# Kernel tuning notes

Measured on AMD Instinct MI355X. Metric: run time of the kernel, lower is better.

## Reference

```python
import jax, jax.numpy as jnp
import numpy as np

N_NODES = 100000
N_EDGES = 1600000
NFEAT = 128
NHID = 128
NCLASS = 40


def gcn_conv(x, W, b, src, dst, n_nodes):
    """PyG-style GCNConv: x' = D^{-1/2}(A+I)D^{-1/2} (x W) + b."""
    h = x @ W  # [N, out]
    loop = jnp.arange(n_nodes, dtype=src.dtype)
    s = jnp.concatenate([src, loop])  # add self-loops
    d = jnp.concatenate([dst, loop])
    deg = jax.ops.segment_sum(jnp.ones_like(s, dtype=h.dtype), d, num_segments=n_nodes)
    dinv = jnp.where(deg > 0, jax.lax.rsqrt(deg), 0.0)
    norm = dinv[s] * dinv[d]  # [E+N]
    msg = h[s] * norm[:, None]  # gather + scale
    out = jax.ops.segment_sum(msg, d, num_segments=n_nodes)  # scatter-add
    return out + b


def setup_inputs() -> dict:
    key = jax.random.key(0)
    ks = jax.random.split(key, 6)
    x = jax.random.normal(ks[0], (N_NODES, NFEAT), dtype=jnp.float32)
    edge_index = jax.random.randint(ks[1], (2, N_EDGES), 0, N_NODES, dtype=jnp.int64)
    sc1 = 1.0 / np.sqrt(NFEAT)
    sc2 = 1.0 / np.sqrt(NHID)
    W1 = jax.random.normal(ks[2], (NFEAT, NHID), dtype=jnp.float32) * sc1
    b1 = jnp.zeros((NHID,), dtype=jnp.float32)
    Wm = jax.random.normal(ks[3], (NHID, NHID), dtype=jnp.float32) * sc2
    bm = jnp.zeros((NHID,), dtype=jnp.float32)
    W2 = jax.random.normal(ks[4], (NHID, NCLASS), dtype=jnp.float32) * sc2
    b2 = jnp.zeros((NCLASS,), dtype=jnp.float32)
    return {"x": x, "edge_index": edge_index, "W1": W1, "b1": b1,
            "Wm": Wm, "bm": bm, "W2": W2, "b2": b2}


def reference(x, edge_index, W1, b1, Wm, bm, W2, b2):
    # StandGCNX forward, eval mode (dropout = identity)
    src, dst = edge_index[0], edge_index[1]
    n = x.shape[0]
    h = jax.nn.relu(gcn_conv(x, W1, b1, src, dst, n))
    h = jax.nn.relu(gcn_conv(h, Wm, bm, src, dst, n))
    out = gcn_conv(h, W2, b2, src, dst, n)
    return out
```

## Files before the change

### kernel.cpp

```cpp
#include <hip/hip_runtime.h>
#include <hip/hip_bf16.h>

typedef __attribute__((ext_vector_type(8))) short bf16x8;
typedef __attribute__((ext_vector_type(4))) float f32x4;

__device__ __forceinline__ ushort bf16rne(float f) {
    uint u = __float_as_uint(f);
    return (ushort)((u + 0x7fffu + ((u >> 16) & 1u)) >> 16);
}
__device__ __forceinline__ void unpack2(uint p, float& a, float& b) {
    a = __uint_as_float(p << 16);
    b = __uint_as_float(p & 0xffff0000u);
}


__global__ __launch_bounds__(256) void k_bhist(const int* __restrict__ dst,
                                               int* __restrict__ bcnt, int E) {
    __shared__ int hist[512];
    int t = threadIdx.x;
    hist[t] = 0; hist[t + 256] = 0;
    __syncthreads();
    int off = blockIdx.x * 4096;
    int cnt = min(4096, E - off);
    for (int i = t; i < cnt; i += 256) atomicAdd(&hist[dst[off + i] >> 8], 1);
    __syncthreads();
    if (hist[t]) atomicAdd(&bcnt[t], hist[t]);
    if (hist[t + 256]) atomicAdd(&bcnt[t + 256], hist[t + 256]);
}

__global__ void k_bscan(const int* __restrict__ bcnt, int* __restrict__ bbase,
                        int* __restrict__ bcur, int nbuck) {
    __shared__ int s[512];
    int t = threadIdx.x;
    s[t] = (t < nbuck) ? bcnt[t] : 0;
    __syncthreads();
    for (int d = 1; d < 512; d <<= 1) {
        int u = (t >= d) ? s[t - d] : 0;
        __syncthreads();
        if (t >= d) s[t] += u;
        __syncthreads();
    }
    int excl = (t == 0) ? 0 : s[t - 1];
    bbase[t] = excl;
    if (t < nbuck) bcur[t] = excl;
    if (t == 511) bbase[512] = s[511];
}

__global__ __launch_bounds__(256) void k_binpack(const int* __restrict__ src,
                                                 const int* __restrict__ dst,
                                                 int* __restrict__ bcur,
                                                 uint* __restrict__ pairbuf,
                                                 int E, int nbuck) {
    __shared__ int hist[512];
    __shared__ int scn[512];
    __shared__ int cur[512];
    __shared__ int gbase[512];
    __shared__ uint sorted[4096];
    int t = threadIdx.x;
    int off = blockIdx.x * 4096;
    int cnt = min(4096, E - off);

    hist[t] = 0; hist[t + 256] = 0;
    __syncthreads();
    for (int i = t; i < cnt; i += 256) {
        int b = dst[off + i] >> 8;
        atomicAdd(&hist[b], 1);
    }
    __syncthreads();
    scn[t] = hist[t]; scn[t + 256] = hist[t + 256];
    __syncthreads();
    for (int d = 1; d < 256; d <<= 1) {
        int u0 = (t >= d) ? scn[t - d] : 0;
        int u1 = (t >= d) ? scn[256 + t - d] : 0;
        __syncthreads();
        if (t >= d) { scn[t] += u0; scn[256 + t] += u1; }
        __syncthreads();
    }
    int tot0 = scn[255];
    scn[256 + t] += tot0;
    __syncthreads();
    cur[t] = (t == 0) ? 0 : scn[t - 1];
    cur[t + 256] = scn[t + 255];
    if (t < nbuck && hist[t] > 0) gbase[t] = atomicAdd(&bcur[t], hist[t]);
    int t2 = t + 256;
    if (t2 < nbuck && hist[t2] > 0) gbase[t2] = atomicAdd(&bcur[t2], hist[t2]);
    __syncthreads();
    for (int i = t; i < cnt; i += 256) {
        int d = dst[off + i];
        int s = src[off + i];
        int b = d >> 8;
        int pos = atomicAdd(&cur[b], 1);
        sorted[pos] = ((uint)(d & 255) << 24) | (uint)s;
    }
    __syncthreads();
    int wid = t >> 6, lane = t & 63;
    for (int b = wid; b < nbuck; b += 4) {
        int n = hist[b];
        if (n == 0) continue;
        int ls = (b == 0) ? 0 : scn[b - 1];
        int gb = gbase[b];
        for (int j = lane; j < n; j += 64)
            pairbuf[gb + j] = sorted[ls + j];
    }
}

#define CSR_CAP 5632
__global__ __launch_bounds__(256) void k_csrbuild(const uint* __restrict__ pairbuf,
                                                  const int* __restrict__ bbase,
                                                  int* __restrict__ rowptr,
                                                  float* __restrict__ dinv,
                                                  int* __restrict__ csr,
                                                  int N, int nbuck) {
    __shared__ int lhist[256];
    __shared__ int scn[256];
    __shared__ int lcur[256];
    __shared__ int lcsr[CSR_CAP];
    int b = blockIdx.x;
    int base = b << 8;
    int nn = min(256, N - base);
    int lo = bbase[b], hi = bbase[b + 1];
    int cnt = hi - lo;
    int t = threadIdx.x;
    lhist[t] = 0;
    __syncthreads();
    for (int i = t; i < cnt; i += 256) atomicAdd(&lhist[pairbuf[lo + i] >> 24], 1);
    __syncthreads();
    int mydeg = lhist[t];
    scn[t] = mydeg;
    __syncthreads();
    for (int d = 1; d < 256; d <<= 1) {
        int u = (t >= d) ? scn[t - d] : 0;
        __syncthreads();
        if (t >= d) scn[t] += u;
        __syncthreads();
    }
    int excl = (t == 0) ? 0 : scn[t - 1];
    lcur[t] = excl;
    if (t < nn) {
        rowptr[base + t] = lo + excl;
        dinv[base + t] = rsqrtf((float)(mydeg + 1));
    }
    if (b == nbuck - 1 && t == 0) rowptr[N] = hi;
    __syncthreads();
    if (cnt <= CSR_CAP) {
        for (int i = t; i < cnt; i += 256) {
            uint p = pairbuf[lo + i];
            int pos = atomicAdd(&lcur[p >> 24], 1);
            lcsr[pos] = (int)(p & 0xFFFFFFu);
        }
        __syncthreads();
        for (int i = t; i < cnt; i += 256) csr[lo + i] = lcsr[i];
    } else {
        for (int i = t; i < cnt; i += 256) {
            uint p = pairbuf[lo + i];
            int pos = lo + atomicAdd(&lcur[p >> 24], 1);
            csr[pos] = (int)(p & 0xFFFFFFu);
        }
    }
}


__global__ void k_castT_all(const float* __restrict__ W1, const float* __restrict__ Wm,
                            const float* __restrict__ W2, ushort* __restrict__ w1t,
                            ushort* __restrict__ wmt, ushort* __restrict__ w2t) {
    int b = blockIdx.x;
    int t = threadIdx.x;
    if (b < 64) {
        int i = b * 256 + t; int k = i >> 7, n = i & 127;
        w1t[n * 128 + k] = bf16rne(W1[k * 128 + n]);
    } else if (b < 128) {
        int i = (b - 64) * 256 + t; int k = i >> 7, n = i & 127;
        wmt[n * 128 + k] = bf16rne(Wm[k * 128 + n]);
    } else {
        int i = (b - 128) * 256 + t;
        if (i < 6144) {
            int n = i >> 7, k = i & 127;
            w2t[n * 128 + k] = (n < 40) ? bf16rne(W2[k * 40 + n]) : (ushort)0;
        }
    }
}


__global__ __launch_bounds__(256) void k_gemm1(const float* __restrict__ A,
                                               const ushort* __restrict__ Wt,
                                               const float* __restrict__ dinv,
                                               ushort* __restrict__ C, int M) {
    int t = threadIdx.x;
    int wave = t >> 6, lane = t & 63;
    int m16 = lane & 15, quad = lane >> 4;
    int rowA = blockIdx.x * 64 + wave * 16 + m16;
    int rA = min(rowA, M - 1);
    const float4* A4 = (const float4*)A;

    f32x4 acc[8];
#pragma unroll
    for (int i = 0; i < 8; i++) acc[i] = (f32x4){0.f, 0.f, 0.f, 0.f};

#pragma unroll
    for (int it = 0; it < 4; it++) {
        float4 f0 = A4[(size_t)rA * 32 + 8 * it + 2 * quad];
        float4 f1 = A4[(size_t)rA * 32 + 8 * it + 2 * quad + 1];
        bf16x8 af;
        af[0] = (short)bf16rne(f0.x); af[1] = (short)bf16rne(f0.y);
        af[2] = (short)bf16rne(f0.z); af[3] = (short)bf16rne(f0.w);
        af[4] = (short)bf16rne(f1.x); af[5] = (short)bf16rne(f1.y);
        af[6] = (short)bf16rne(f1.z); af[7] = (short)bf16rne(f1.w);
#pragma unroll
        for (int nt = 0; nt < 8; nt++) {
            bf16x8 bfr = *(const bf16x8*)(Wt + (size_t)(nt * 16 + m16) * 128 + it * 32 + quad * 8);
            acc[nt] = __builtin_amdgcn_mfma_f32_16x16x32_bf16(af, bfr, acc[nt], 0, 0, 0);
        }
    }
    int rowBase = blockIdx.x * 64 + wave * 16 + quad * 4;
    float dnv[4];
#pragma unroll
    for (int r = 0; r < 4; r++) dnv[r] = dinv[min(rowBase + r, M - 1)];
#pragma unroll
    for (int nt = 0; nt < 8; nt++) {
        int col = nt * 16 + m16;
#pragma unroll
        for (int r = 0; r < 4; r++) {
            int row = rowBase + r;
            if (row < M) C[(size_t)row * 128 + col] = bf16rne(acc[nt][r] * dnv[r]);
        }
    }
}


template <int NT>
__device__ __forceinline__ void fused_agg_gemm(const ushort* __restrict__ g,
                                               const float* __restrict__ dinv,
                                               const int* __restrict__ rowptr,
                                               const int* __restrict__ csr,
                                               const float* __restrict__ bias,
                                               const ushort* __restrict__ Wt,
                                               ushort* __restrict__ C,
                                               int M, int ccols) {
    int t = threadIdx.x;
    int wave = t >> 6, lane = t & 63;
    int m16 = lane & 15, quad = lane >> 4;
    int node = blockIdx.x * 64 + wave * 16 + m16;
    int nd = min(node, M - 1);
    const uint4* g16 = (const uint4*)g;
    float dn = dinv[nd];

    float a[4][8];
    {
#pragma unroll
        for (int it = 0; it < 4; it++) {
            uint4 p = g16[(size_t)nd * 16 + 4 * it + quad];
            unpack2(p.x, a[it][0], a[it][1]); unpack2(p.y, a[it][2], a[it][3]);
            unpack2(p.z, a[it][4], a[it][5]); unpack2(p.w, a[it][6], a[it][7]);
        }
    }
    int e0 = rowptr[nd], e1 = rowptr[nd + 1];
    int e = e0;
    for (; e + 2 <= e1; e += 2) {
        int s0 = csr[e], s1 = csr[e + 1];
        uint4 p0[4], p1[4];
#pragma unroll
        for (int it = 0; it < 4; it++) p0[it] = g16[(size_t)s0 * 16 + 4 * it + quad];
#pragma unroll
        for (int it = 0; it < 4; it++) p1[it] = g16[(size_t)s1 * 16 + 4 * it + quad];
        float u, v;
#pragma unroll
        for (int it = 0; it < 4; it++) {
            unpack2(p0[it].x, u, v); a[it][0] += u; a[it][1] += v;
            unpack2(p0[it].y, u, v); a[it][2] += u; a[it][3] += v;
            unpack2(p0[it].z, u, v); a[it][4] += u; a[it][5] += v;
            unpack2(p0[it].w, u, v); a[it][6] += u; a[it][7] += v;
            unpack2(p1[it].x, u, v); a[it][0] += u; a[it][1] += v;
            unpack2(p1[it].y, u, v); a[it][2] += u; a[it][3] += v;
            unpack2(p1[it].z, u, v); a[it][4] += u; a[it][5] += v;
            unpack2(p1[it].w, u, v); a[it][6] += u; a[it][7] += v;
        }
    }
    for (; e < e1; e++) {
        int s = csr[e];
        float u, v;
#pragma unroll
        for (int it = 0; it < 4; it++) {
            uint4 p = g16[(size_t)s * 16 + 4 * it + quad];
            unpack2(p.x, u, v); a[it][0] += u; a[it][1] += v;
            unpack2(p.y, u, v); a[it][2] += u; a[it][3] += v;
            unpack2(p.z, u, v); a[it][4] += u; a[it][5] += v;
            unpack2(p.w, u, v); a[it][6] += u; a[it][7] += v;
        }
    }
    const float4* b4 = (const float4*)bias;
    bf16x8 frag[4];
#pragma unroll
    for (int it = 0; it < 4; it++) {
        float4 bb0 = b4[8 * it + 2 * quad];
        float4 bb1 = b4[8 * it + 2 * quad + 1];
        float o0 = fmaxf(a[it][0] * dn + bb0.x, 0.f);
        float o1 = fmaxf(a[it][1] * dn + bb0.y, 0.f);
        float o2 = fmaxf(a[it][2] * dn + bb0.z, 0.f);
        float o3 = fmaxf(a[it][3] * dn + bb0.w, 0.f);
        float o4 = fmaxf(a[it][4] * dn + bb1.x, 0.f);
        float o5 = fmaxf(a[it][5] * dn + bb1.y, 0.f);
        float o6 = fmaxf(a[it][6] * dn + bb1.z, 0.f);
        float o7 = fmaxf(a[it][7] * dn + bb1.w, 0.f);
        frag[it][0] = (short)bf16rne(o0); frag[it][1] = (short)bf16rne(o1);
        frag[it][2] = (short)bf16rne(o2); frag[it][3] = (short)bf16rne(o3);
        frag[it][4] = (short)bf16rne(o4); frag[it][5] = (short)bf16rne(o5);
        frag[it][6] = (short)bf16rne(o6); frag[it][7] = (short)bf16rne(o7);
    }
    f32x4 acc[NT];
#pragma unroll
    for (int i = 0; i < NT; i++) acc[i] = (f32x4){0.f, 0.f, 0.f, 0.f};
#pragma unroll
    for (int it = 0; it < 4; it++) {
#pragma unroll
        for (int nt = 0; nt < NT; nt++) {
            bf16x8 bfr = *(const bf16x8*)(Wt + (size_t)(nt * 16 + m16) * 128 + it * 32 + quad * 8);
            acc[nt] = __builtin_amdgcn_mfma_f32_16x16x32_bf16(frag[it], bfr, acc[nt], 0, 0, 0);
        }
    }
    int rowBase = blockIdx.x * 64 + wave * 16 + quad * 4;
    float dnv[4];
#pragma unroll
    for (int r = 0; r < 4; r++) dnv[r] = dinv[min(rowBase + r, M - 1)];
#pragma unroll
    for (int nt = 0; nt < NT; nt++) {
        int col = nt * 16 + m16;
        if (col >= ccols) continue;
#pragma unroll
        for (int r = 0; r < 4; r++) {
            int row = rowBase + r;
            if (row < M) C[(size_t)row * ccols + col] = bf16rne(acc[nt][r] * dnv[r]);
        }
    }
}

__global__ __launch_bounds__(256) void k_fusedA(const ushort* __restrict__ g,
                                                const float* __restrict__ dinv,
                                                const int* __restrict__ rowptr,
                                                const int* __restrict__ csr,
                                                const float* __restrict__ bias,
                                                const ushort* __restrict__ Wt,
                                                ushort* __restrict__ C, int M) {
    fused_agg_gemm<8>(g, dinv, rowptr, csr, bias, Wt, C, M, 128);
}

__global__ __launch_bounds__(256) void k_fusedB(const ushort* __restrict__ g,
                                                const float* __restrict__ dinv,
                                                const int* __restrict__ rowptr,
                                                const int* __restrict__ csr,
                                                const float* __restrict__ bias,
                                                const ushort* __restrict__ Wt,
                                                ushort* __restrict__ C, int M) {
    fused_agg_gemm<3>(g, dinv, rowptr, csr, bias, Wt, C, M, 40);
}


__global__ __launch_bounds__(256) void k_agg40_b(const ushort* __restrict__ g3,
                                                 const float* __restrict__ dinv,
                                                 const int* __restrict__ rowptr,
                                                 const int* __restrict__ csr,
                                                 const float* __restrict__ bias,
                                                 float* __restrict__ out, int N) {
    int t = threadIdx.x;
    if (t >= 250) return;
    int grp = t / 10;
    int l = t - grp * 10;
    int node = blockIdx.x * 25 + grp;
    if (node >= N) return;
    const uint2* gp = (const uint2*)g3;
    float dn = dinv[node];
    float a0, a1, a2, a3;
    {
        uint2 p = gp[(size_t)node * 10 + l];
        unpack2(p.x, a0, a1);
        unpack2(p.y, a2, a3);
    }
    int e0 = rowptr[node], e1 = rowptr[node + 1];
    int e = e0;
    for (; e + 4 <= e1; e += 4) {
        int s0 = csr[e], s1 = csr[e + 1], s2 = csr[e + 2], s3 = csr[e + 3];
        uint2 p0 = gp[(size_t)s0 * 10 + l];
        uint2 p1 = gp[(size_t)s1 * 10 + l];
        uint2 p2 = gp[(size_t)s2 * 10 + l];
        uint2 p3 = gp[(size_t)s3 * 10 + l];
        float u, v;
        unpack2(p0.x, u, v); a0 += u; a1 += v;
        unpack2(p0.y, u, v); a2 += u; a3 += v;
        unpack2(p1.x, u, v); a0 += u; a1 += v;
        unpack2(p1.y, u, v); a2 += u; a3 += v;
        unpack2(p2.x, u, v); a0 += u; a1 += v;
        unpack2(p2.y, u, v); a2 += u; a3 += v;
        unpack2(p3.x, u, v); a0 += u; a1 += v;
        unpack2(p3.y, u, v); a2 += u; a3 += v;
    }
    for (; e < e1; e++) {
        int s = csr[e];
        uint2 p = gp[(size_t)s * 10 + l];
        float u, v;
        unpack2(p.x, u, v); a0 += u; a1 += v;
        unpack2(p.y, u, v); a2 += u; a3 += v;
    }
    float4 bb = ((const float4*)bias)[l];
    float4 o;
    o.x = a0 * dn + bb.x;
    o.y = a1 * dn + bb.y;
    o.z = a2 * dn + bb.z;
    o.w = a3 * dn + bb.w;
    ((float4*)out)[(size_t)node * 10 + l] = o;
}


extern "C" void kernel_launch(void* const* d_in, const int* in_sizes, int n_in,
                              void* d_out, int out_size, void* d_ws, size_t ws_size,
                              hipStream_t stream) {
    const float* x  = (const float*)d_in[0];
    const int* eidx = (const int*)d_in[1];
    const float* W1 = (const float*)d_in[2];
    const float* b1 = (const float*)d_in[3];
    const float* Wm = (const float*)d_in[4];
    const float* bm = (const float*)d_in[5];
    const float* W2 = (const float*)d_in[6];
    const float* b2 = (const float*)d_in[7];
    float* out = (float*)d_out;

    int N = in_sizes[0] / 128;
    int E = in_sizes[1] / 2;
    const int* src = eidx;
    const int* dst = eidx + E;
    int nbuck = (N + 255) >> 8;

    char* ws = (char*)d_ws;
    size_t off = 0;
    auto alloc = [&](size_t bytes) -> void* {
        void* p = ws + off;
        off += (bytes + 255) & ~(size_t)255;
        return p;
    };
    float*  dinv    = (float*)alloc((size_t)N * 4);
    int*    rowptr  = (int*)alloc(((size_t)N + 1) * 4);
    int*    csr     = (int*)alloc((size_t)E * 4);
    uint*   pairbuf = (uint*)alloc((size_t)E * 4);
    int*    bcnt    = (int*)alloc(512 * 4);
    int*    bbase   = (int*)alloc(513 * 4);
    int*    bcur    = (int*)alloc(512 * 4);
    ushort* w1t     = (ushort*)alloc(128 * 128 * 2);
    ushort* wmt     = (ushort*)alloc(128 * 128 * 2);
    ushort* w2t     = (ushort*)alloc(48 * 128 * 2);
    ushort* gbuf    = (ushort*)alloc((size_t)N * 128 * 2);
    ushort* gbuf2   = (ushort*)alloc((size_t)N * 128 * 2);
    ushort* g3      = (ushort*)alloc((size_t)N * 40 * 2);

    hipMemsetAsync(bcnt, 0, 512 * 4, stream);
    k_bhist<<<(E + 4095) / 4096, 256, 0, stream>>>(dst, bcnt, E);
    k_bscan<<<1, 512, 0, stream>>>(bcnt, bbase, bcur, nbuck);
    k_binpack<<<(E + 4095) / 4096, 256, 0, stream>>>(src, dst, bcur, pairbuf, E, nbuck);
    k_csrbuild<<<nbuck, 256, 0, stream>>>(pairbuf, bbase, rowptr, dinv, csr, N, nbuck);
    k_castT_all<<<152, 256, 0, stream>>>(W1, Wm, W2, w1t, wmt, w2t);

    int gblk = (N + 63) / 64;
    k_gemm1<<<gblk, 256, 0, stream>>>(x, w1t, dinv, gbuf, N);
    k_fusedA<<<gblk, 256, 0, stream>>>(gbuf, dinv, rowptr, csr, b1, wmt, gbuf2, N);
    k_fusedB<<<gblk, 256, 0, stream>>>(gbuf2, dinv, rowptr, csr, bm, w2t, g3, N);
    k_agg40_b<<<(N + 24) / 25, 256, 0, stream>>>(g3, dinv, rowptr, csr, b2, out, N);
}
```

Measured before the change: 415.8 us.

## Restructure fused aggregation to gather whole rows per 16-lane group via LDS staging

The aggregation phase now assigns each 16-lane group a full 128-feature row: one uint4 per lane, so each neighbor gather is a contiguous 256-byte segment instead of strided pieces spread across quads. Each group processes 4 nodes in sequence and unrolls the edge loop by 4. Results are written as bf16 into a shared-memory tile, followed by a barrier, and the MFMA phase reads its A fragments from LDS. This is meant to improve gather coalescing and cut per-thread register pressure. The cost is the LDS round trip, a block-level sync, and a serial loop over 4 nodes per group.

```diff
diff --git a/kernel.cpp b/kernel.cpp
--- a/kernel.cpp
+++ b/kernel.cpp
@@ -236,85 +236,89 @@
                                                const ushort* __restrict__ Wt,
                                                ushort* __restrict__ C,
                                                int M, int ccols) {
-    int t = threadIdx.x;
+    __shared__ ushort hs[64][136];
+    int t = threadIdx.x;
+    int grp = t >> 4;
+    int l = t & 15;
+    const uint4* g16 = (const uint4*)g;
+    float4 bb0 = ((const float4*)bias)[2 * l];
+    float4 bb1 = ((const float4*)bias)[2 * l + 1];
+
+#pragma unroll
+    for (int q = 0; q < 4; q++) {
+        int node = blockIdx.x * 64 + grp * 4 + q;
+        int nd = min(node, M - 1);
+        float dn = dinv[nd];
+        float a[8];
+        {
+            uint4 p = g16[(size_t)nd * 16 + l];
+            unpack2(p.x, a[0], a[1]); unpack2(p.y, a[2], a[3]);
+            unpack2(p.z, a[4], a[5]); unpack2(p.w, a[6], a[7]);
+        }
+        int e0 = rowptr[nd], e1 = rowptr[nd + 1];
+        int e = e0;
+        for (; e + 4 <= e1; e += 4) {
+            int s0 = csr[e], s1 = csr[e + 1], s2 = csr[e + 2], s3 = csr[e + 3];
+            uint4 p0 = g16[(size_t)s0 * 16 + l];
+            uint4 p1 = g16[(size_t)s1 * 16 + l];
+            uint4 p2 = g16[(size_t)s2 * 16 + l];
+            uint4 p3 = g16[(size_t)s3 * 16 + l];
+            float u, v;
+            unpack2(p0.x, u, v); a[0] += u; a[1] += v;
+            unpack2(p0.y, u, v); a[2] += u; a[3] += v;
+            unpack2(p0.z, u, v); a[4] += u; a[5] += v;
+            unpack2(p0.w, u, v); a[6] += u; a[7] += v;
+            unpack2(p1.x, u, v); a[0] += u; a[1] += v;
+            unpack2(p1.y, u, v); a[2] += u; a[3] += v;
+            unpack2(p1.z, u, v); a[4] += u; a[5] += v;
+            unpack2(p1.w, u, v); a[6] += u; a[7] += v;
+            unpack2(p2.x, u, v); a[0] += u; a[1] += v;
+            unpack2(p2.y, u, v); a[2] += u; a[3] += v;
+            unpack2(p2.z, u, v); a[4] += u; a[5] += v;
+            unpack2(p2.w, u, v); a[6] += u; a[7] += v;
+            unpack2(p3.x, u, v); a[0] += u; a[1] += v;
+            unpack2(p3.y, u, v); a[2] += u; a[3] += v;
+            unpack2(p3.z, u, v); a[4] += u; a[5] += v;
+            unpack2(p3.w, u, v); a[6] += u; a[7] += v;
+        }
+        for (; e < e1; e++) {
+            int s = csr[e];
+            uint4 p = g16[(size_t)s * 16 + l];
+            float u, v;
+            unpack2(p.x, u, v); a[0] += u; a[1] += v;
+            unpack2(p.y, u, v); a[2] += u; a[3] += v;
+            unpack2(p.z, u, v); a[4] += u; a[5] += v;
+            unpack2(p.w, u, v); a[6] += u; a[7] += v;
+        }
+        float o0 = fmaxf(a[0] * dn + bb0.x, 0.f);
+        float o1 = fmaxf(a[1] * dn + bb0.y, 0.f);
+        float o2 = fmaxf(a[2] * dn + bb0.z, 0.f);
+        float o3 = fmaxf(a[3] * dn + bb0.w, 0.f);
+        float o4 = fmaxf(a[4] * dn + bb1.x, 0.f);
+        float o5 = fmaxf(a[5] * dn + bb1.y, 0.f);
+        float o6 = fmaxf(a[6] * dn + bb1.z, 0.f);
+        float o7 = fmaxf(a[7] * dn + bb1.w, 0.f);
+        uint4 qv;
+        qv.x = (uint)bf16rne(o0) | ((uint)bf16rne(o1) << 16);
+        qv.y = (uint)bf16rne(o2) | ((uint)bf16rne(o3) << 16);
+        qv.z = (uint)bf16rne(o4) | ((uint)bf16rne(o5) << 16);
+        qv.w = (uint)bf16rne(o6) | ((uint)bf16rne(o7) << 16);
+        *(uint4*)&hs[grp * 4 + q][l * 8] = qv;
+    }
+    __syncthreads();
+
     int wave = t >> 6, lane = t & 63;
     int m16 = lane & 15, quad = lane >> 4;
-    int node = blockIdx.x * 64 + wave * 16 + m16;
-    int nd = min(node, M - 1);
-    const uint4* g16 = (const uint4*)g;
-    float dn = dinv[nd];
-
-    float a[4][8];
-    {
-#pragma unroll
-        for (int it = 0; it < 4; it++) {
-            uint4 p = g16[(size_t)nd * 16 + 4 * it + quad];
-            unpack2(p.x, a[it][0], a[it][1]); unpack2(p.y, a[it][2], a[it][3]);
-            unpack2(p.z, a[it][4], a[it][5]); unpack2(p.w, a[it][6], a[it][7]);
-        }
-    }
-    int e0 = rowptr[nd], e1 = rowptr[nd + 1];
-    int e = e0;
-    for (; e + 2 <= e1; e += 2) {
-        int s0 = csr[e], s1 = csr[e + 1];
-        uint4 p0[4], p1[4];
-#pragma unroll
-        for (int it = 0; it < 4; it++) p0[it] = g16[(size_t)s0 * 16 + 4 * it + quad];
-#pragma unroll
-        for (int it = 0; it < 4; it++) p1[it] = g16[(size_t)s1 * 16 + 4 * it + quad];
-        float u, v;
-#pragma unroll
-        for (int it = 0; it < 4; it++) {
-            unpack2(p0[it].x, u, v); a[it][0] += u; a[it][1] += v;
-            unpack2(p0[it].y, u, v); a[it][2] += u; a[it][3] += v;
-            unpack2(p0[it].z, u, v); a[it][4] += u; a[it][5] += v;
-            unpack2(p0[it].w, u, v); a[it][6] += u; a[it][7] += v;
-            unpack2(p1[it].x, u, v); a[it][0] += u; a[it][1] += v;
-            unpack2(p1[it].y, u, v); a[it][2] += u; a[it][3] += v;
-            unpack2(p1[it].z, u, v); a[it][4] += u; a[it][5] += v;
-            unpack2(p1[it].w, u, v); a[it][6] += u; a[it][7] += v;
-        }
-    }
-    for (; e < e1; e++) {
-        int s = csr[e];
-        float u, v;
-#pragma unroll
-        for (int it = 0; it < 4; it++) {
-            uint4 p = g16[(size_t)s * 16 + 4 * it + quad];
-            unpack2(p.x, u, v); a[it][0] += u; a[it][1] += v;
-            unpack2(p.y, u, v); a[it][2] += u; a[it][3] += v;
-            unpack2(p.z, u, v); a[it][4] += u; a[it][5] += v;
-            unpack2(p.w, u, v); a[it][6] += u; a[it][7] += v;
-        }
-    }
-    const float4* b4 = (const float4*)bias;
-    bf16x8 frag[4];
+    f32x4 acc[NT];
+#pragma unroll
+    for (int i = 0; i < NT; i++) acc[i] = (f32x4){0.f, 0.f, 0.f, 0.f};
 #pragma unroll
     for (int it = 0; it < 4; it++) {
-        float4 bb0 = b4[8 * it + 2 * quad];
-        float4 bb1 = b4[8 * it + 2 * quad + 1];
-        float o0 = fmaxf(a[it][0] * dn + bb0.x, 0.f);
-        float o1 = fmaxf(a[it][1] * dn + bb0.y, 0.f);
-        float o2 = fmaxf(a[it][2] * dn + bb0.z, 0.f);
-        float o3 = fmaxf(a[it][3] * dn + bb0.w, 0.f);
-        float o4 = fmaxf(a[it][4] * dn + bb1.x, 0.f);
-        float o5 = fmaxf(a[it][5] * dn + bb1.y, 0.f);
-        float o6 = fmaxf(a[it][6] * dn + bb1.z, 0.f);
-        float o7 = fmaxf(a[it][7] * dn + bb1.w, 0.f);
-        frag[it][0] = (short)bf16rne(o0); frag[it][1] = (short)bf16rne(o1);
-        frag[it][2] = (short)bf16rne(o2); frag[it][3] = (short)bf16rne(o3);
-        frag[it][4] = (short)bf16rne(o4); frag[it][5] = (short)bf16rne(o5);
-        frag[it][6] = (short)bf16rne(o6); frag[it][7] = (short)bf16rne(o7);
-    }
-    f32x4 acc[NT];
-#pragma unroll
-    for (int i = 0; i < NT; i++) acc[i] = (f32x4){0.f, 0.f, 0.f, 0.f};
-#pragma unroll
-    for (int it = 0; it < 4; it++) {
+        bf16x8 af = *(const bf16x8*)&hs[wave * 16 + m16][it * 32 + quad * 8];
 #pragma unroll
         for (int nt = 0; nt < NT; nt++) {
             bf16x8 bfr = *(const bf16x8*)(Wt + (size_t)(nt * 16 + m16) * 128 + it * 32 + quad * 8);
-            acc[nt] = __builtin_amdgcn_mfma_f32_16x16x32_bf16(frag[it], bfr, acc[nt], 0, 0, 0);
+            acc[nt] = __builtin_amdgcn_mfma_f32_16x16x32_bf16(af, bfr, acc[nt], 0, 0, 0);
         }
     }
     int rowBase = blockIdx.x * 64 + wave * 16 + quad * 4;
```

Result: no change. 411.2 us (-1.1%).

## Split fused aggregate-GEMM into feature-sliced aggregation and separate GEMM kernels

Applied to the files above, without the earlier changes.

Stores intermediate node features in a column-sliced layout (8 slices of 16 bf16 features per node), so each aggregation block gathers only one 32-byte slice per neighbor and its working set per slice is far smaller. This is meant to improve L2 hit rates for the random neighbor gathers. The fused aggregate+GEMM kernels are replaced by separate aggregation and MFMA GEMM kernels. The cost is extra kernel launches and an extra round trip of the hidden features through memory.

```diff
diff --git a/kernel.cpp b/kernel.cpp
--- a/kernel.cpp
+++ b/kernel.cpp
@@ -181,6 +181,7 @@
 }
 
 
+
 __global__ __launch_bounds__(256) void k_gemm1(const float* __restrict__ A,
                                                const ushort* __restrict__ Wt,
                                                const float* __restrict__ dinv,
@@ -217,104 +218,100 @@
     for (int r = 0; r < 4; r++) dnv[r] = dinv[min(rowBase + r, M - 1)];
 #pragma unroll
     for (int nt = 0; nt < 8; nt++) {
-        int col = nt * 16 + m16;
 #pragma unroll
         for (int r = 0; r < 4; r++) {
             int row = rowBase + r;
-            if (row < M) C[(size_t)row * 128 + col] = bf16rne(acc[nt][r] * dnv[r]);
-        }
-    }
-}
-
-
-template <int NT>
-__device__ __forceinline__ void fused_agg_gemm(const ushort* __restrict__ g,
-                                               const float* __restrict__ dinv,
-                                               const int* __restrict__ rowptr,
-                                               const int* __restrict__ csr,
-                                               const float* __restrict__ bias,
-                                               const ushort* __restrict__ Wt,
-                                               ushort* __restrict__ C,
-                                               int M, int ccols) {
+            if (row < M) C[((size_t)nt * M + row) * 16 + m16] = bf16rne(acc[nt][r] * dnv[r]);
+        }
+    }
+}
+
+
+__global__ __launch_bounds__(256) void k_aggS(const ushort* __restrict__ g,
+                                              const float* __restrict__ dinv,
+                                              const int* __restrict__ rowptr,
+                                              const int* __restrict__ csr,
+                                              const float* __restrict__ bias,
+                                              ushort* __restrict__ hout, int N) {
+    int s = blockIdx.x & 7;
+    int chunk = blockIdx.x >> 3;
+    int t = threadIdx.x;
+    int grp = t >> 2;
+    int l4 = t & 3;
+    int node = chunk * 64 + grp;
+    if (node >= N) return;
+    const ushort* gs = g + (size_t)s * N * 16;
+    float dn = dinv[node];
+    float4 bb = *(const float4*)(bias + s * 16 + l4 * 4);
+    float a0, a1, a2, a3;
+    {
+        uint2 p = *(const uint2*)(gs + (size_t)node * 16 + l4 * 4);
+        unpack2(p.x, a0, a1);
+        unpack2(p.y, a2, a3);
+    }
+    int e0 = rowptr[node], e1 = rowptr[node + 1];
+    int e = e0;
+    for (; e + 4 <= e1; e += 4) {
+        int s0 = __builtin_nontemporal_load(csr + e);
+        int s1 = __builtin_nontemporal_load(csr + e + 1);
+        int s2 = __builtin_nontemporal_load(csr + e + 2);
+        int s3 = __builtin_nontemporal_load(csr + e + 3);
+        uint2 p0 = *(const uint2*)(gs + (size_t)s0 * 16 + l4 * 4);
+        uint2 p1 = *(const uint2*)(gs + (size_t)s1 * 16 + l4 * 4);
+        uint2 p2 = *(const uint2*)(gs + (size_t)s2 * 16 + l4 * 4);
+        uint2 p3 = *(const uint2*)(gs + (size_t)s3 * 16 + l4 * 4);
+        float u, v;
+        unpack2(p0.x, u, v); a0 += u; a1 += v;
+        unpack2(p0.y, u, v); a2 += u; a3 += v;
+        unpack2(p1.x, u, v); a0 += u; a1 += v;
+        unpack2(p1.y, u, v); a2 += u; a3 += v;
+        unpack2(p2.x, u, v); a0 += u; a1 += v;
+        unpack2(p2.y, u, v); a2 += u; a3 += v;
+        unpack2(p3.x, u, v); a0 += u; a1 += v;
+        unpack2(p3.y, u, v); a2 += u; a3 += v;
+    }
+    for (; e < e1; e++) {
+        int s0 = __builtin_nontemporal_load(csr + e);
+        uint2 p = *(const uint2*)(gs + (size_t)s0 * 16 + l4 * 4);
+        float u, v;
+        unpack2(p.x, u, v); a0 += u; a1 += v;
+        unpack2(p.y, u, v); a2 += u; a3 += v;
+    }
+    float o0 = fmaxf(a0 * dn + bb.x, 0.f);
+    float o1 = fmaxf(a1 * dn + bb.y, 0.f);
+    float o2 = fmaxf(a2 * dn + bb.z, 0.f);
+    float o3 = fmaxf(a3 * dn + bb.w, 0.f);
+    uint2 q;
+    q.x = (uint)bf16rne(o0) | ((uint)bf16rne(o1) << 16);
+    q.y = (uint)bf16rne(o2) | ((uint)bf16rne(o3) << 16);
+    *(uint2*)(hout + ((size_t)s * N + node) * 16 + l4 * 4) = q;
+}
+
+
+template <int NT, bool SLICED_OUT>
+__device__ __forceinline__ void gemm_sliced(const ushort* __restrict__ A,
+                                            const ushort* __restrict__ Wt,
+                                            const float* __restrict__ dinv,
+                                            ushort* __restrict__ C, int M, int ccols) {
     int t = threadIdx.x;
     int wave = t >> 6, lane = t & 63;
     int m16 = lane & 15, quad = lane >> 4;
-    int node = blockIdx.x * 64 + wave * 16 + m16;
-    int nd = min(node, M - 1);
-    const uint4* g16 = (const uint4*)g;
-    float dn = dinv[nd];
-
-    float a[4][8];
-    {
-#pragma unroll
-        for (int it = 0; it < 4; it++) {
-            uint4 p = g16[(size_t)nd * 16 + 4 * it + quad];
-            unpack2(p.x, a[it][0], a[it][1]); unpack2(p.y, a[it][2], a[it][3]);
-            unpack2(p.z, a[it][4], a[it][5]); unpack2(p.w, a[it][6], a[it][7]);
-        }
-    }
-    int e0 = rowptr[nd], e1 = rowptr[nd + 1];
-    int e = e0;
-    for (; e + 2 <= e1; e += 2) {
-        int s0 = csr[e], s1 = csr[e + 1];
-        uint4 p0[4], p1[4];
-#pragma unroll
-        for (int it = 0; it < 4; it++) p0[it] = g16[(size_t)s0 * 16 + 4 * it + quad];
-#pragma unroll
-        for (int it = 0; it < 4; it++) p1[it] = g16[(size_t)s1 * 16 + 4 * it + quad];
-        float u, v;
-#pragma unroll
-        for (int it = 0; it < 4; it++) {
-            unpack2(p0[it].x, u, v); a[it][0] += u; a[it][1] += v;
-            unpack2(p0[it].y, u, v); a[it][2] += u; a[it][3] += v;
-            unpack2(p0[it].z, u, v); a[it][4] += u; a[it][5] += v;
-            unpack2(p0[it].w, u, v); a[it][6] += u; a[it][7] += v;
-            unpack2(p1[it].x, u, v); a[it][0] += u; a[it][1] += v;
-            unpack2(p1[it].y, u, v); a[it][2] += u; a[it][3] += v;
-            unpack2(p1[it].z, u, v); a[it][4] += u; a[it][5] += v;
-            unpack2(p1[it].w, u, v); a[it][6] += u; a[it][7] += v;
-        }
-    }
-    for (; e < e1; e++) {
-        int s = csr[e];
-        float u, v;
-#pragma unroll
-        for (int it = 0; it < 4; it++) {
-            uint4 p = g16[(size_t)s * 16 + 4 * it + quad];
-            unpack2(p.x, u, v); a[it][0] += u; a[it][1] += v;
-            unpack2(p.y, u, v); a[it][2] += u; a[it][3] += v;
-            unpack2(p.z, u, v); a[it][4] += u; a[it][5] += v;
-            unpack2(p.w, u, v); a[it][6] += u; a[it][7] += v;
-        }
-    }
-    const float4* b4 = (const float4*)bias;
-    bf16x8 frag[4];
+    int rowA = blockIdx.x * 64 + wave * 16 + m16;
+    int rA = min(rowA, M - 1);
+
+    f32x4 acc[NT];
+#pragma unroll
+    for (int i = 0; i < NT; i++) acc[i] = (f32x4){0.f, 0.f, 0.f, 0.f};
+
 #pragma unroll
     for (int it = 0; it < 4; it++) {
-        float4 bb0 = b4[8 * it + 2 * quad];
-        float4 bb1 = b4[8 * it + 2 * quad + 1];
-        float o0 = fmaxf(a[it][0] * dn + bb0.x, 0.f);
-        float o1 = fmaxf(a[it][1] * dn + bb0.y, 0.f);
-        float o2 = fmaxf(a[it][2] * dn + bb0.z, 0.f);
-        float o3 = fmaxf(a[it][3] * dn + bb0.w, 0.f);
-        float o4 = fmaxf(a[it][4] * dn + bb1.x, 0.f);
-        float o5 = fmaxf(a[it][5] * dn + bb1.y, 0.f);
-        float o6 = fmaxf(a[it][6] * dn + bb1.z, 0.f);
-        float o7 = fmaxf(a[it][7] * dn + bb1.w, 0.f);
-        frag[it][0] = (short)bf16rne(o0); frag[it][1] = (short)bf16rne(o1);
-        frag[it][2] = (short)bf16rne(o2); frag[it][3] = (short)bf16rne(o3);
-        frag[it][4] = (short)bf16rne(o4); frag[it][5] = (short)bf16rne(o5);
-        frag[it][6] = (short)bf16rne(o6); frag[it][7] = (short)bf16rne(o7);
-    }
-    f32x4 acc[NT];
-#pragma unroll
-    for (int i = 0; i < NT; i++) acc[i] = (f32x4){0.f, 0.f, 0.f, 0.f};
-#pragma unroll
-    for (int it = 0; it < 4; it++) {
+        int k = it * 32 + quad * 8;
+        int sl = k >> 4, ko = k & 15;
+        bf16x8 af = *(const bf16x8*)(A + ((size_t)sl * M + rA) * 16 + ko);
 #pragma unroll
         for (int nt = 0; nt < NT; nt++) {
             bf16x8 bfr = *(const bf16x8*)(Wt + (size_t)(nt * 16 + m16) * 128 + it * 32 + quad * 8);
-            acc[nt] = __builtin_amdgcn_mfma_f32_16x16x32_bf16(frag[it], bfr, acc[nt], 0, 0, 0);
+            acc[nt] = __builtin_amdgcn_mfma_f32_16x16x32_bf16(af, bfr, acc[nt], 0, 0, 0);
         }
     }
     int rowBase = blockIdx.x * 64 + wave * 16 + quad * 4;
@@ -324,33 +321,32 @@
 #pragma unroll
     for (int nt = 0; nt < NT; nt++) {
         int col = nt * 16 + m16;
-        if (col >= ccols) continue;
 #pragma unroll
         for (int r = 0; r < 4; r++) {
             int row = rowBase + r;
-            if (row < M) C[(size_t)row * ccols + col] = bf16rne(acc[nt][r] * dnv[r]);
-        }
-    }
-}
-
-__global__ __launch_bounds__(256) void k_fusedA(const ushort* __restrict__ g,
-                                                const float* __restrict__ dinv,
-                                                const int* __restrict__ rowptr,
-                                                const int* __restrict__ csr,
-                                                const float* __restrict__ bias,
-                                                const ushort* __restrict__ Wt,
-                                                ushort* __restrict__ C, int M) {
-    fused_agg_gemm<8>(g, dinv, rowptr, csr, bias, Wt, C, M, 128);
-}
-
-__global__ __launch_bounds__(256) void k_fusedB(const ushort* __restrict__ g,
-                                                const float* __restrict__ dinv,
-                                                const int* __restrict__ rowptr,
-                                                const int* __restrict__ csr,
-                                                const float* __restrict__ bias,
-                                                const ushort* __restrict__ Wt,
-                                                ushort* __restrict__ C, int M) {
-    fused_agg_gemm<3>(g, dinv, rowptr, csr, bias, Wt, C, M, 40);
+            if (row >= M) continue;
+            ushort val = bf16rne(acc[nt][r] * dnv[r]);
+            if (SLICED_OUT) {
+                C[((size_t)nt * M + row) * 16 + m16] = val;
+            } else if (col < ccols) {
+                C[(size_t)row * ccols + col] = val;
+            }
+        }
+    }
+}
+
+__global__ __launch_bounds__(256) void k_gemmS(const ushort* __restrict__ A,
+                                               const ushort* __restrict__ Wt,
+                                               const float* __restrict__ dinv,
+                                               ushort* __restrict__ C, int M) {
+    gemm_sliced<8, true>(A, Wt, dinv, C, M, 128);
+}
+
+__global__ __launch_bounds__(256) void k_gemm3(const ushort* __restrict__ A,
+                                               const ushort* __restrict__ Wt,
+                                               const float* __restrict__ dinv,
+                                               ushort* __restrict__ C, int M) {
+    gemm_sliced<3, false>(A, Wt, dinv, C, M, 40);
 }
 
 
@@ -445,8 +441,8 @@
     ushort* w1t     = (ushort*)alloc(128 * 128 * 2);
     ushort* wmt     = (ushort*)alloc(128 * 128 * 2);
     ushort* w2t     = (ushort*)alloc(48 * 128 * 2);
-    ushort* gbuf    = (ushort*)alloc((size_t)N * 128 * 2);
-    ushort* gbuf2   = (ushort*)alloc((size_t)N * 128 * 2);
+    ushort* gbufS   = (ushort*)alloc((size_t)N * 128 * 2);
+    ushort* hbufS   = (ushort*)alloc((size_t)N * 128 * 2);
     ushort* g3      = (ushort*)alloc((size_t)N * 40 * 2);
 
     hipMemsetAsync(bcnt, 0, 512 * 4, stream);
@@ -456,9 +452,12 @@
     k_csrbuild<<<nbuck, 256, 0, stream>>>(pairbuf, bbase, rowptr, dinv, csr, N, nbuck);
     k_castT_all<<<152, 256, 0, stream>>>(W1, Wm, W2, w1t, wmt, w2t);
 
-    int gblk = (N + 63) / 64;
-    k_gemm1<<<gblk, 256, 0, stream>>>(x, w1t, dinv, gbuf, N);
-    k_fusedA<<<gblk, 256, 0, stream>>>(gbuf, dinv, rowptr, csr, b1, wmt, gbuf2, N);
-    k_fusedB<<<gblk, 256, 0, stream>>>(gbuf2, dinv, rowptr, csr, bm, w2t, g3, N);
+    int gblk64 = (N + 63) / 64;
+    int aggGrid = ((N + 63) / 64) * 8;
+    k_gemm1<<<gblk64, 256, 0, stream>>>(x, w1t, dinv, gbufS, N);
+    k_aggS<<<aggGrid, 256, 0, stream>>>(gbufS, dinv, rowptr, csr, b1, hbufS, N);
+    k_gemmS<<<gblk64, 256, 0, stream>>>(hbufS, wmt, dinv, gbufS, N);
+    k_aggS<<<aggGrid, 256, 0, stream>>>(gbufS, dinv, rowptr, csr, bm, hbufS, N);
+    k_gemm3<<<gblk64, 256, 0, stream>>>(hbufS, w2t, dinv, g3, N);
     k_agg40_b<<<(N + 24) / 25, 256, 0, stream>>>(g3, dinv, rowptr, csr, b2, out, N);
 }
```

After: 556.8 us. 33.9% more time.
